# Performance work log

Measured on AMD Instinct MI355X. Metric: run time of the kernel, lower is better.

The kernel has to match this reference:

```python
import jax, jax.numpy as jnp
import numpy as np

L, D, H, DH, S, B, V = 8, 1024, 16, 64, 1024, 4, 32000
EPS = 1e-5


def layernorm(x, s, b):
    m = x.mean(-1, keepdims=True)
    v = ((x - m) ** 2).mean(-1, keepdims=True)
    return (x - m) * jax.lax.rsqrt(v + EPS) * s + b


def setup_inputs() -> dict:
    key = jax.random.key(0)
    ks = jax.random.split(key, 12)
    sd = 0.02
    inp = {
        'idx': jax.random.randint(ks[0], (B, S), 0, V),
        'tok_emb': jax.random.normal(ks[1], (V, D), jnp.float32) * sd,
        'pos_emb': jax.random.normal(ks[2], (S, D), jnp.float32) * sd,
        'ln1_s': jnp.ones((L, D), jnp.float32),
        'ln1_b': jnp.zeros((L, D), jnp.float32),
        'wq': jax.random.normal(ks[3], (L, H, D, DH), jnp.float32) * sd,
        'wk': jax.random.normal(ks[4], (L, H, D, DH), jnp.float32) * sd,
        'wv': jax.random.normal(ks[5], (L, H, D, DH), jnp.float32) * sd,
        'wproj': jax.random.normal(ks[6], (L, D, D), jnp.float32) * sd,  # stored [D_in, D_out]
        'ln2_s': jnp.ones((L, D), jnp.float32),
        'ln2_b': jnp.zeros((L, D), jnp.float32),
        'w1': jax.random.normal(ks[7], (L, D, 4 * D), jnp.float32) * sd,
        'b1': jnp.zeros((L, 4 * D), jnp.float32),
        'w2': jax.random.normal(ks[8], (L, 4 * D, D), jnp.float32) * sd,
        'b2': jnp.zeros((L, D), jnp.float32),
        'lnf_s': jnp.ones((D,), jnp.float32),
        'lnf_b': jnp.zeros((D,), jnp.float32),
        'lm_w': jax.random.normal(ks[9], (D, V), jnp.float32) * sd,  # stored [D_in, V]
        'lm_b': jnp.zeros((V,), jnp.float32),
    }
    return inp


def reference(idx, tok_emb, pos_emb, ln1_s, ln1_b, wq, wk, wv, wproj,
              ln2_s, ln2_b, w1, b1, w2, b2, lnf_s, lnf_b, lm_w, lm_b):
    T = idx.shape[1]
    x = tok_emb[idx] + pos_emb[:T]  # [B,T,D]
    mask = jnp.tril(jnp.ones((T, T), bool))
    scale = DH ** -0.5
    for l in range(L):  # fixed small layer count
        h = layernorm(x, ln1_s[l], ln1_b[l])
        q = jnp.einsum('bsd,hde->bhse', h, wq[l])
        k = jnp.einsum('bsd,hde->bhse', h, wk[l])
        v = jnp.einsum('bsd,hde->bhse', h, wv[l])
        att = jnp.einsum('bhse,bhte->bhst', q, k) * scale
        att = jnp.where(mask, att, -jnp.inf)
        att = jax.nn.softmax(att, axis=-1)  # dropout=0.0 -> identity
        o = jnp.einsum('bhst,bhte->bhse', att, v)
        o = o.transpose(0, 2, 1, 3).reshape(x.shape)  # concat heads: [B,T,H*DH]
        x = x + o @ wproj[l]
        h2 = layernorm(x, ln2_s[l], ln2_b[l])
        x = x + jax.nn.relu(h2 @ w1[l] + b1[l]) @ w2[l] + b2[l]
    x = layernorm(x, lnf_s, lnf_b)
    logits = x @ lm_w + lm_b  # [B,T,V]
    return logits
```

## Files before the change

kernel.cpp:

```cpp
#include <hip/hip_runtime.h>
#include <hip/hip_bf16.h>

#define LL 8
#define DD 1024
#define HH 16
#define DHH 64
#define SS 1024
#define BB 4
#define VV 32000
#define MM (BB * SS)

typedef unsigned short u16;
typedef __attribute__((ext_vector_type(8))) short short8v;
typedef __attribute__((ext_vector_type(4))) float f32x4;
typedef unsigned int __attribute__((address_space(1))) guint;
typedef unsigned int __attribute__((address_space(3))) luint;

__device__ __forceinline__ float bf2f_lo(unsigned u) { return __uint_as_float(u << 16); }
__device__ __forceinline__ u16 f2bf(float f) {
  unsigned x = __float_as_uint(f);
  return (u16)((x + 0x7fffu + ((x >> 16) & 1u)) >> 16);
}

__global__ __launch_bounds__(256) void embed_kernel(
    const int* __restrict__ idx, const float* __restrict__ tok,
    const float* __restrict__ pos, float* __restrict__ x) {
  int i = blockIdx.x * blockDim.x + threadIdx.x;
  int elem = i * 4;
  int row = elem / DD;
  int d = elem % DD;
  int s = row % SS;
  int t = idx[row];
  float4 tv = *(const float4*)(tok + (size_t)t * DD + d);
  float4 pv = *(const float4*)(pos + (size_t)s * DD + d);
  tv.x += pv.x; tv.y += pv.y; tv.z += pv.z; tv.w += pv.w;
  *(float4*)(x + (size_t)elem) = tv;
}

__global__ __launch_bounds__(256) void ln_bf16_kernel(
    const float* __restrict__ x, const float* __restrict__ sc,
    const float* __restrict__ bi, u16* __restrict__ out) {
  const int row = blockIdx.x;
  const int tid = threadIdx.x;
  __shared__ float red[4];
  float4 v = ((const float4*)(x + (size_t)row * DD))[tid];
  float s = v.x + v.y + v.z + v.w;
  #pragma unroll
  for (int off = 32; off; off >>= 1) s += __shfl_down(s, off);
  if ((tid & 63) == 0) red[tid >> 6] = s;
  __syncthreads();
  float mean = (red[0] + red[1] + red[2] + red[3]) * (1.f / DD);
  float dx = v.x - mean, dy = v.y - mean, dz = v.z - mean, dw = v.w - mean;
  float vs = dx * dx + dy * dy + dz * dz + dw * dw;
  __syncthreads();
  #pragma unroll
  for (int off = 32; off; off >>= 1) vs += __shfl_down(vs, off);
  if ((tid & 63) == 0) red[tid >> 6] = vs;
  __syncthreads();
  float var = (red[0] + red[1] + red[2] + red[3]) * (1.f / DD);
  float rstd = rsqrtf(var + 1e-5f);
  float4 s4 = ((const float4*)sc)[tid];
  float4 b4 = ((const float4*)bi)[tid];
  ushort4 o;
  o.x = f2bf(dx * rstd * s4.x + b4.x);
  o.y = f2bf(dy * rstd * s4.y + b4.y);
  o.z = f2bf(dz * rstd * s4.z + b4.z);
  o.w = f2bf(dw * rstd * s4.w + b4.w);
  *(ushort4*)(out + (size_t)row * DD + tid * 4) = o;
}

template <bool HEADW>
__global__ __launch_bounds__(256) void convT_kernel(
    const float* __restrict__ W, u16* __restrict__ BT, int K, int N,
    size_t lstride) {
  __shared__ float tile[32][33];
  const int n0 = blockIdx.x * 32, k0 = blockIdx.y * 32, l = blockIdx.z;
  const int tx = threadIdx.x & 31, ty = threadIdx.x >> 5;
  const float* Wl;
  int ld;
  if (HEADW) {
    const int h = n0 >> 6;
    Wl = W + ((size_t)(l * HH + h) * K) * 64 + (n0 & 63);
    ld = 64;
  } else {
    Wl = W + (size_t)l * K * N + n0;
    ld = N;
  }
  #pragma unroll
  for (int i = 0; i < 4; ++i)
    tile[ty + 8 * i][tx] = Wl[(size_t)(k0 + ty + 8 * i) * ld + tx];
  __syncthreads();
  u16* out = BT + (size_t)l * lstride;
  #pragma unroll
  for (int i = 0; i < 4; ++i)
    out[(size_t)(n0 + ty + 8 * i) * K + k0 + tx] = f2bf(tile[tx][ty + 8 * i]);
}

template <bool BIAS, bool RELU, bool RESID, bool OBF16>
__global__ __launch_bounds__(256) void gemm_mfma(
    const u16* __restrict__ A, const u16* __restrict__ BT,
    const float* __restrict__ bias, const float* __restrict__ resid,
    void* __restrict__ Cv, int M, int N, int K) {
  __shared__ u16 As[128 * 64];
  __shared__ u16 Bs[128 * 64];
  const int tid = threadIdx.x;
  const int lane = tid & 63, wave = tid >> 6;
  const int m0 = blockIdx.x * 128, n0 = blockIdx.y * 128;
  const int wr = (wave >> 1) * 64, wc = (wave & 1) * 64;
  const int srow = tid >> 3;
  const int scol = (((tid & 7) ^ (srow & 7)) * 8);
  const u16* Ag = A + (size_t)(m0 + srow) * K + scol;
  const u16* Bg = BT + (size_t)(n0 + srow) * K + scol;

  f32x4 acc[4][4] = {};
  for (int k0 = 0; k0 < K; k0 += 64) {
    #pragma unroll
    for (int c = 0; c < 4; ++c) {
      __builtin_amdgcn_global_load_lds(
          (const guint*)(Ag + k0 + (size_t)c * 32 * K),
          (luint*)(As + c * 2048 + tid * 8), 16, 0, 0);
      __builtin_amdgcn_global_load_lds(
          (const guint*)(Bg + k0 + (size_t)c * 32 * K),
          (luint*)(Bs + c * 2048 + tid * 8), 16, 0, 0);
    }
    __syncthreads();
    #pragma unroll
    for (int kk = 0; kk < 64; kk += 32) {
      const int chA = (((kk >> 3) | (lane >> 4)) ^ (lane & 7)) * 8;
      short8v av[4], bv[4];
      #pragma unroll
      for (int i = 0; i < 4; ++i)
        av[i] = *(const short8v*)(As + (wr + i * 16 + (lane & 15)) * 64 + chA);
      #pragma unroll
      for (int j = 0; j < 4; ++j)
        bv[j] = *(const short8v*)(Bs + (wc + j * 16 + (lane & 15)) * 64 + chA);
      #pragma unroll
      for (int i = 0; i < 4; ++i)
        #pragma unroll
        for (int j = 0; j < 4; ++j)
          acc[i][j] = __builtin_amdgcn_mfma_f32_16x16x32_bf16(av[i], bv[j], acc[i][j], 0, 0, 0);
    }
    __syncthreads();
  }
  #pragma unroll
  for (int i = 0; i < 4; ++i) {
    #pragma unroll
    for (int j = 0; j < 4; ++j) {
      const int col = n0 + wc + j * 16 + (lane & 15);
      #pragma unroll
      for (int r = 0; r < 4; ++r) {
        const int row = m0 + wr + i * 16 + (lane >> 4) * 4 + r;
        float v = acc[i][j][r];
        if (BIAS) v += bias[col];
        if (RELU) v = fmaxf(v, 0.f);
        if (RESID) v += resid[(size_t)row * N + col];
        if (OBF16)
          ((u16*)Cv)[(size_t)row * N + col] = f2bf(v);
        else
          ((float*)Cv)[(size_t)row * N + col] = v;
      }
    }
  }
}

#define LDA_(BUF, KH, F) \
  (*(const short8v*)&As[BUF][KH][(wm * 128 + (F) * 16 + (lane & 15)) * 32 + rg])
#define LDB_(BUF, KH, NF) \
  (*(const short8v*)&Bs[BUF][KH][(wn * 64 + (NF) * 16 + (lane & 15)) * 32 + rg])
#define LDS_A(S0,S1,S2,S3, BUF, KH, FB) { \
  S0 = LDA_(BUF, KH, (FB) + 0); S1 = LDA_(BUF, KH, (FB) + 1); \
  S2 = LDA_(BUF, KH, (FB) + 2); S3 = LDA_(BUF, KH, (FB) + 3); }
#define LDS_B(S0,S1,S2,S3, BUF, KH) { \
  S0 = LDB_(BUF, KH, 0); S1 = LDB_(BUF, KH, 1); \
  S2 = LDB_(BUF, KH, 2); S3 = LDB_(BUF, KH, 3); }
#define STAGE_A(BUF, KH, KT) do { \
  __builtin_amdgcn_global_load_lds((const guint*)(Abase + (KT) * 64 + (KH) * 32), \
      (luint*)(&As[BUF][KH][tid * 8]), 16, 0, 0); \
  __builtin_amdgcn_global_load_lds((const guint*)(Abase + (size_t)128 * K + (KT) * 64 + (KH) * 32), \
      (luint*)(&As[BUF][KH][(tid + 512) * 8]), 16, 0, 0); \
} while (0)
#define STAGE_B(BUF, KH, KT) do { \
  __builtin_amdgcn_global_load_lds((const guint*)(Bbase + (KT) * 64 + (KH) * 32), \
      (luint*)(&Bs[BUF][KH][tid * 8]), 16, 0, 0); \
  __builtin_amdgcn_global_load_lds((const guint*)(Bbase + (size_t)128 * K + (KT) * 64 + (KH) * 32), \
      (luint*)(&Bs[BUF][KH][(tid + 512) * 8]), 16, 0, 0); \
} while (0)
#define MROW(F, AQ, B0,B1,B2,B3) \
  acc[F][0] = __builtin_amdgcn_mfma_f32_16x16x32_bf16(AQ, B0, acc[F][0], 0, 0, 0); \
  acc[F][1] = __builtin_amdgcn_mfma_f32_16x16x32_bf16(AQ, B1, acc[F][1], 0, 0, 0); \
  acc[F][2] = __builtin_amdgcn_mfma_f32_16x16x32_bf16(AQ, B2, acc[F][2], 0, 0, 0); \
  acc[F][3] = __builtin_amdgcn_mfma_f32_16x16x32_bf16(AQ, B3, acc[F][3], 0, 0, 0);
#define MFMA16S(FB, A0,A1,A2,A3, B0,B1,B2,B3) \
  MROW((FB) + 0, A0, B0,B1,B2,B3) MROW((FB) + 1, A1, B0,B1,B2,B3) \
  MROW((FB) + 2, A2, B0,B1,B2,B3) MROW((FB) + 3, A3, B0,B1,B2,B3)
#define BARRIER __builtin_amdgcn_s_barrier()
#define MEMFENCE asm volatile("" ::: "memory")

#define TILE4(CUR, KT, ST1, ST2, V1STR, V3STR, LD4, LGK4STR) { \
  const int cur_ = (CUR); \
   \
  MEMFENCE; \
  LDS_A(aN0,aN1,aN2,aN3, cur_, 0, 4); \
  if (ST1) { STAGE_A(cur_ ^ 1, 1, (KT) + 1); } \
  asm volatile("s_waitcnt " V1STR ::: "memory"); \
  asm volatile("s_waitcnt lgkmcnt(4)" ::: "memory"); \
  BARRIER; \
  __builtin_amdgcn_s_setprio(1); \
  MFMA16S(0, aP0,aP1,aP2,aP3, bP0,bP1,bP2,bP3); \
  __builtin_amdgcn_s_setprio(0); \
   \
  MEMFENCE; \
  LDS_A(aP0,aP1,aP2,aP3, cur_, 1, 0); \
  LDS_B(bN0,bN1,bN2,bN3, cur_, 1); \
  if (ST1) { STAGE_B(cur_ ^ 1, 1, (KT) + 1); } \
  asm volatile("s_waitcnt lgkmcnt(8)" ::: "memory"); \
  BARRIER; \
  __builtin_amdgcn_s_setprio(1); \
  MFMA16S(4, aN0,aN1,aN2,aN3, bP0,bP1,bP2,bP3); \
  __builtin_amdgcn_s_setprio(0); \
   \
  MEMFENCE; \
  LDS_A(aN0,aN1,aN2,aN3, cur_, 1, 4); \
  if (ST2) { STAGE_A(cur_, 0, (KT) + 2); } \
  asm volatile("s_waitcnt " V3STR ::: "memory"); \
  asm volatile("s_waitcnt lgkmcnt(4)" ::: "memory"); \
  BARRIER; \
  __builtin_amdgcn_s_setprio(1); \
  MFMA16S(0, aP0,aP1,aP2,aP3, bN0,bN1,bN2,bN3); \
  __builtin_amdgcn_s_setprio(0); \
   \
  MEMFENCE; \
  if (LD4) { LDS_A(aP0,aP1,aP2,aP3, cur_ ^ 1, 0, 0); \
             LDS_B(bP0,bP1,bP2,bP3, cur_ ^ 1, 0); } \
  if (ST2) { STAGE_B(cur_, 0, (KT) + 2); } \
  asm volatile("s_waitcnt " LGK4STR ::: "memory"); \
  BARRIER; \
  __builtin_amdgcn_s_setprio(1); \
  MFMA16S(4, aN0,aN1,aN2,aN3, bN0,bN1,bN2,bN3); \
  __builtin_amdgcn_s_setprio(0); \
}

template <bool BIAS, bool RELU, bool RESID, bool OBF16>
__global__ __launch_bounds__(512, 2) void gemm8(
    const u16* __restrict__ A, const u16* __restrict__ BT,
    const float* __restrict__ bias, const float* __restrict__ resid,
    void* __restrict__ Cv, int M, int N, int K) {
  __shared__ u16 As[2][2][8192];
  __shared__ u16 Bs[2][2][8192];
  const int tid = threadIdx.x;
  const int lane = tid & 63, wave = tid >> 6;
  const int wm = wave >> 2, wn = wave & 3;
  const int nwg = gridDim.x;
  const int bid = blockIdx.x;
  const int wg = ((nwg & 7) == 0) ? ((bid & 7) * (nwg >> 3) + (bid >> 3)) : bid;
  const int nmt = M >> 8;
  const int m0 = (wg % nmt) * 256;
  const int n0 = (wg / nmt) * 256;
  const int NT = K >> 6;
  const int sr = tid >> 2;
  const int ssc = (((tid & 3) ^ ((tid >> 3) & 3)) * 8);
  const u16* Abase = A + (size_t)(m0 + sr) * K + ssc;
  const u16* Bbase = BT + (size_t)(n0 + sr) * K + ssc;
  const int rg = (((lane >> 4) ^ ((lane >> 1) & 3)) * 8);

  f32x4 acc[8][4] = {};
  short8v aP0, aP1, aP2, aP3, aN0, aN1, aN2, aN3;
  short8v bP0, bP1, bP2, bP3, bN0, bN1, bN2, bN3;

  STAGE_A(0, 0, 0); STAGE_B(0, 0, 0);
  STAGE_A(0, 1, 0); STAGE_B(0, 1, 0);
  STAGE_A(1, 0, 1); STAGE_B(1, 0, 1);
  asm volatile("s_waitcnt vmcnt(8)" ::: "memory");
  BARRIER;
  MEMFENCE;
  LDS_A(aP0,aP1,aP2,aP3, 0, 0, 0);
  LDS_B(bP0,bP1,bP2,bP3, 0, 0);

  int kt = 0;
  for (; kt < NT - 2; ++kt) {
    TILE4(kt & 1, kt, true, true, "vmcnt(6)", "vmcnt(6)", true, "lgkmcnt(8)");
  }
  TILE4(kt & 1, kt, true, false, "vmcnt(6)", "vmcnt(4)", true, "lgkmcnt(8)");
  ++kt;
  TILE4(kt & 1, kt, false, false, "vmcnt(0)", "vmcnt(0)", false, "lgkmcnt(0)");

  #pragma unroll
  for (int f = 0; f < 8; ++f) {
    #pragma unroll
    for (int n = 0; n < 4; ++n) {
      const int col = n0 + wn * 64 + n * 16 + (lane & 15);
      #pragma unroll
      for (int r = 0; r < 4; ++r) {
        const int row = m0 + wm * 128 + f * 16 + (lane >> 4) * 4 + r;
        float v = acc[f][n][r];
        if (BIAS) v += bias[col];
        if (RELU) v = fmaxf(v, 0.f);
        if (RESID) v += resid[(size_t)row * N + col];
        if (OBF16)
          ((u16*)Cv)[(size_t)row * N + col] = f2bf(v);
        else
          ((float*)Cv)[(size_t)row * N + col] = v;
      }
    }
  }
}

__global__ __launch_bounds__(256) void gemm_fb(
    const u16* __restrict__ A, const float* __restrict__ B,
    const float* __restrict__ bias, float* __restrict__ C, int M, int N, int K) {
  __shared__ alignas(16) float Asm[16][68];
  __shared__ alignas(16) float Bsm[16][68];
  const int tid = threadIdx.x;
  const int tx = tid & 15, ty = tid >> 4;
  const int m0 = blockIdx.y * 64, n0 = blockIdx.x * 64;
  const int ar = tid >> 2, ac = (tid & 3) * 4;
  const int br = tid >> 4, bc = (tid & 15) * 4;
  float acc[4][4] = {};
  for (int k0 = 0; k0 < K; k0 += 16) {
    ushort4 au = *(const ushort4*)(A + (size_t)(m0 + ar) * K + k0 + ac);
    float4 bv = *(const float4*)(B + (size_t)(k0 + br) * N + n0 + bc);
    Asm[ac + 0][ar] = bf2f_lo(au.x);
    Asm[ac + 1][ar] = bf2f_lo(au.y);
    Asm[ac + 2][ar] = bf2f_lo(au.z);
    Asm[ac + 3][ar] = bf2f_lo(au.w);
    *(float4*)&Bsm[br][bc] = bv;
    __syncthreads();
    #pragma unroll
    for (int kk = 0; kk < 16; ++kk) {
      float4 a = *(const float4*)&Asm[kk][ty * 4];
      float4 b = *(const float4*)&Bsm[kk][tx * 4];
      acc[0][0] += a.x * b.x; acc[0][1] += a.x * b.y; acc[0][2] += a.x * b.z; acc[0][3] += a.x * b.w;
      acc[1][0] += a.y * b.x; acc[1][1] += a.y * b.y; acc[1][2] += a.y * b.z; acc[1][3] += a.y * b.w;
      acc[2][0] += a.z * b.x; acc[2][1] += a.z * b.y; acc[2][2] += a.z * b.z; acc[2][3] += a.z * b.w;
      acc[3][0] += a.w * b.x; acc[3][1] += a.w * b.y; acc[3][2] += a.w * b.z; acc[3][3] += a.w * b.w;
    }
    __syncthreads();
  }
  #pragma unroll
  for (int i = 0; i < 4; ++i) {
    const int m = m0 + ty * 4 + i;
    #pragma unroll
    for (int j = 0; j < 4; ++j) {
      const int n = n0 + tx * 4 + j;
      C[(size_t)m * N + n] = acc[i][j] + bias[n];
    }
  }
}

__global__ __launch_bounds__(256) void attn_mfma(
    const u16* __restrict__ qk, const u16* __restrict__ vt,
    u16* __restrict__ o) {
  __shared__ alignas(16) u16 Ksh[64 * 64];
  __shared__ alignas(16) u16 Vsh[64 * 64];
  __shared__ unsigned Plds[4][16 * 41];
  __shared__ float bcast[4][16];
  const int tid = threadIdx.x;
  const int lane = tid & 63, wave = tid >> 6;
  const int g = lane >> 4, qi = lane & 15;
  const int qt = blockIdx.x, h = blockIdx.y, b = blockIdx.z;
  const int q0w = qt * 64 + wave * 16;
  const int qloc = wave * 16 + qi;

  short8v qf0, qf1;
  {
    const u16* qp = qk + ((size_t)b * SS + q0w + qi) * 2048 + h * DHH + g * 8;
    qf0 = *(const short8v*)qp;
    qf1 = *(const short8v*)(qp + 32);
  }

  f32x4 oacc[4] = {};
  float mrow = -1e30f, lrow = 0.f;

  for (int kt = 0; kt <= qt; ++kt) {
    __syncthreads();
    #pragma unroll
    for (int u = 0; u < 2; ++u) {
      const int unit = tid + 256 * u;
      const int row = unit >> 3, ch = unit & 7;
      const int sch = ch ^ (row & 7);
      __builtin_amdgcn_global_load_lds(
          (const guint*)(qk + ((size_t)b * SS + kt * 64 + row) * 2048 + 1024 + h * DHH + sch * 8),
          (luint*)(Ksh + unit * 8), 16, 0, 0);
      __builtin_amdgcn_global_load_lds(
          (const guint*)(vt + ((size_t)(h * DHH + row)) * MM + b * SS + kt * 64 + sch * 8),
          (luint*)(Vsh + unit * 8), 16, 0, 0);
    }
    __syncthreads();

    f32x4 st[4] = {};
    #pragma unroll
    for (int t = 0; t < 4; ++t) {
      const int row = t * 16 + qi;
      const int swz = (row & 7) << 4;
      short8v kf0 = *(const short8v*)(Ksh + row * 64 + (((g * 16) ^ swz) >> 1));
      short8v kf1 = *(const short8v*)(Ksh + row * 64 + (((64 + g * 16) ^ swz) >> 1));
      st[t] = __builtin_amdgcn_mfma_f32_16x16x32_bf16(kf0, qf0, st[t], 0, 0, 0);
      st[t] = __builtin_amdgcn_mfma_f32_16x16x32_bf16(kf1, qf1, st[t], 0, 0, 0);
    }

    if (kt == qt) {
      #pragma unroll
      for (int t = 0; t < 4; ++t)
        #pragma unroll
        for (int r = 0; r < 4; ++r)
          if (t * 16 + 4 * g + r > qloc) st[t][r] = -1e30f;
    }

    float mt = st[0][0];
    #pragma unroll
    for (int t = 0; t < 4; ++t)
      #pragma unroll
      for (int r = 0; r < 4; ++r) mt = fmaxf(mt, st[t][r]);
    mt = fmaxf(mt, __shfl_xor(mt, 16));
    mt = fmaxf(mt, __shfl_xor(mt, 32));
    const float mnew = fmaxf(mrow, mt * 0.125f);
    const float corr = __expf(mrow - mnew);
    float pl = 0.f;
    #pragma unroll
    for (int t = 0; t < 4; ++t) {
      #pragma unroll
      for (int r2 = 0; r2 < 2; ++r2) {
        float plo = __expf(fmaf(st[t][2 * r2], 0.125f, -mnew));
        float phi = __expf(fmaf(st[t][2 * r2 + 1], 0.125f, -mnew));
        pl += plo + phi;
        Plds[wave][qi * 41 + 8 * t + 2 * g + r2] =
            (unsigned)f2bf(plo) | ((unsigned)f2bf(phi) << 16);
      }
    }
    pl += __shfl_xor(pl, 16);
    pl += __shfl_xor(pl, 32);
    lrow = lrow * corr + pl;
    mrow = mnew;

    if (g == 0) bcast[wave][qi] = corr;
    float c0 = bcast[wave][g * 4 + 0];
    float c1 = bcast[wave][g * 4 + 1];
    float c2 = bcast[wave][g * 4 + 2];
    float c3 = bcast[wave][g * 4 + 3];
    #pragma unroll
    for (int dvt = 0; dvt < 4; ++dvt) {
      oacc[dvt][0] *= c0; oacc[dvt][1] *= c1;
      oacc[dvt][2] *= c2; oacc[dvt][3] *= c3;
    }

    union U8 { unsigned u[4]; short8v s8; };
    U8 pa0, pa1;
    #pragma unroll
    for (int c = 0; c < 4; ++c) {
      pa0.u[c] = Plds[wave][qi * 41 + g * 4 + c];
      pa1.u[c] = Plds[wave][qi * 41 + 16 + g * 4 + c];
    }
    #pragma unroll
    for (int dvt = 0; dvt < 4; ++dvt) {
      const int row = dvt * 16 + qi;
      const int swz = (row & 7) << 4;
      short8v v0 = *(const short8v*)(Vsh + row * 64 + (((g * 16) ^ swz) >> 1));
      short8v v1 = *(const short8v*)(Vsh + row * 64 + (((64 + g * 16) ^ swz) >> 1));
      oacc[dvt] = __builtin_amdgcn_mfma_f32_16x16x32_bf16(pa0.s8, v0, oacc[dvt], 0, 0, 0);
      oacc[dvt] = __builtin_amdgcn_mfma_f32_16x16x32_bf16(pa1.s8, v1, oacc[dvt], 0, 0, 0);
    }
  }

  if (g == 0) bcast[wave][qi] = 1.f / lrow;
  float i0 = bcast[wave][g * 4 + 0];
  float i1 = bcast[wave][g * 4 + 1];
  float i2 = bcast[wave][g * 4 + 2];
  float i3 = bcast[wave][g * 4 + 3];
  #pragma unroll
  for (int dvt = 0; dvt < 4; ++dvt) {
    const int col = h * DHH + dvt * 16 + qi;
    o[((size_t)b * SS + q0w + g * 4 + 0) * DD + col] = f2bf(oacc[dvt][0] * i0);
    o[((size_t)b * SS + q0w + g * 4 + 1) * DD + col] = f2bf(oacc[dvt][1] * i1);
    o[((size_t)b * SS + q0w + g * 4 + 2) * DD + col] = f2bf(oacc[dvt][2] * i2);
    o[((size_t)b * SS + q0w + g * 4 + 3) * DD + col] = f2bf(oacc[dvt][3] * i3);
  }
}

extern "C" void kernel_launch(void* const* d_in, const int* in_sizes, int n_in,
                              void* d_out, int out_size, void* d_ws, size_t ws_size,
                              hipStream_t stream) {
  const int* idx = (const int*)d_in[0];
  const float* tok_emb = (const float*)d_in[1];
  const float* pos_emb = (const float*)d_in[2];
  const float* ln1_s = (const float*)d_in[3];
  const float* ln1_b = (const float*)d_in[4];
  const float* wq = (const float*)d_in[5];
  const float* wk = (const float*)d_in[6];
  const float* wv = (const float*)d_in[7];
  const float* wproj = (const float*)d_in[8];
  const float* ln2_s = (const float*)d_in[9];
  const float* ln2_b = (const float*)d_in[10];
  const float* w1 = (const float*)d_in[11];
  const float* b1 = (const float*)d_in[12];
  const float* w2 = (const float*)d_in[13];
  const float* b2 = (const float*)d_in[14];
  const float* lnf_s = (const float*)d_in[15];
  const float* lnf_b = (const float*)d_in[16];
  const float* lm_w = (const float*)d_in[17];
  const float* lm_b = (const float*)d_in[18];

  const size_t MD = (size_t)MM * DD;

  u16* sc0 = (u16*)d_out;
  u16* BTqk = sc0;
  u16* BTv = BTqk + (size_t)LL * 2048 * DD;
  u16* BTp = BTv + (size_t)LL * DD * DD;
  u16* BTw1 = BTp + (size_t)LL * DD * DD;
  u16* BTw2 = BTw1 + (size_t)LL * DD * 4 * DD;
  u16* qkb = BTw2 + (size_t)LL * DD * 4 * DD;
  u16* vtb = qkb + (size_t)MM * 2048;
  u16* ob = vtb + MD;
  u16* tmp = ob + MD;

  float* x = (float*)d_ws;
  u16* h = (u16*)((char*)d_ws + MD * 4);
  u16* BTlm = (u16*)((char*)d_ws + MD * 4 + MD * 2);
  const bool big_ws = ws_size >= (MD * 4 + MD * 2 + (size_t)VV * DD * 2);

  const dim3 blk(256);

  convT_kernel<true><<<dim3(DD / 32, DD / 32, LL), blk, 0, stream>>>(
      wq, BTqk, DD, DD, (size_t)2048 * DD);
  convT_kernel<true><<<dim3(DD / 32, DD / 32, LL), blk, 0, stream>>>(
      wk, BTqk + (size_t)DD * DD, DD, DD, (size_t)2048 * DD);
  convT_kernel<true><<<dim3(DD / 32, DD / 32, LL), blk, 0, stream>>>(
      wv, BTv, DD, DD, (size_t)DD * DD);
  convT_kernel<false><<<dim3(DD / 32, DD / 32, LL), blk, 0, stream>>>(
      wproj, BTp, DD, DD, (size_t)DD * DD);
  convT_kernel<false><<<dim3(4 * DD / 32, DD / 32, LL), blk, 0, stream>>>(
      w1, BTw1, DD, 4 * DD, (size_t)DD * 4 * DD);
  convT_kernel<false><<<dim3(DD / 32, 4 * DD / 32, LL), blk, 0, stream>>>(
      w2, BTw2, 4 * DD, DD, (size_t)4 * DD * DD);
  if (big_ws)
    convT_kernel<false><<<dim3(VV / 32, DD / 32, 1), blk, 0, stream>>>(
        lm_w, BTlm, DD, VV, (size_t)VV * DD);

  embed_kernel<<<(MM * DD / 4 + 255) / 256, blk, 0, stream>>>(idx, tok_emb, pos_emb, x);

  for (int l = 0; l < LL; ++l) {
    ln_bf16_kernel<<<MM, blk, 0, stream>>>(x, ln1_s + l * DD, ln1_b + l * DD, h);
    gemm8<false, false, false, true><<<dim3((MM / 256) * (2048 / 256)), dim3(512), 0, stream>>>(
        h, BTqk + (size_t)l * 2048 * DD, nullptr, nullptr, qkb, MM, 2048, DD);
    gemm_mfma<false, false, false, true><<<dim3(DD / 128, MM / 128), blk, 0, stream>>>(
        BTv + (size_t)l * DD * DD, h, nullptr, nullptr, vtb, DD, MM, DD);
    attn_mfma<<<dim3(SS / 64, HH, BB), blk, 0, stream>>>(qkb, vtb, ob);
    gemm_mfma<false, false, true, false><<<dim3(MM / 128, DD / 128), blk, 0, stream>>>(
        ob, BTp + (size_t)l * DD * DD, nullptr, x, x, MM, DD, DD);
    ln_bf16_kernel<<<MM, blk, 0, stream>>>(x, ln2_s + l * DD, ln2_b + l * DD, h);
    gemm8<true, true, false, true><<<dim3((MM / 256) * (4 * DD / 256)), dim3(512), 0, stream>>>(
        h, BTw1 + (size_t)l * DD * 4 * DD, b1 + (size_t)l * 4 * DD, nullptr, tmp,
        MM, 4 * DD, DD);
    gemm_mfma<true, false, true, false><<<dim3(MM / 128, DD / 128), blk, 0, stream>>>(
        tmp, BTw2 + (size_t)l * 4 * DD * DD, b2 + (size_t)l * DD, x, x, MM, DD, 4 * DD);
  }

  ln_bf16_kernel<<<MM, blk, 0, stream>>>(x, lnf_s, lnf_b, h);
  if (big_ws) {
    gemm8<true, false, false, false><<<dim3((MM / 256) * (VV / 256)), dim3(512), 0, stream>>>(
        h, BTlm, lm_b, nullptr, (float*)d_out, MM, VV, DD);
  } else {
    gemm_fb<<<dim3(VV / 64, MM / 64), blk, 0, stream>>>(
        h, lm_w, lm_b, (float*)d_out, MM, VV, DD);
  }
}
```

Measured before the change: 2.714 ms.

## Fuse QKV projection into one GEMM, transpose V separately, add nontemporal stores

Concatenates the Q, K and V weight transposes into a single 3072-wide B matrix. The projection now runs as one gemm8 launch instead of a gemm8 plus a separate gemm_mfma for V. A new transpose_v kernel builds the V^T layout that attention expects, and the attention kernel now reads Q and K with a 3072 stride. Separately, nontemporal stores are added for the FFN1 output, the LM-head logits and the fallback GEMM output, to reduce cache pollution; the extra transpose pass costs additional memory traffic.

After: 2.621 ms. 3.4% less time.

```diff
diff --git a/kernel.cpp b/kernel.cpp
--- a/kernel.cpp
+++ b/kernel.cpp
@@ -94,6 +94,20 @@
   #pragma unroll
   for (int i = 0; i < 4; ++i)
     out[(size_t)(n0 + ty + 8 * i) * K + k0 + tx] = f2bf(tile[tx][ty + 8 * i]);
+}
+
+__global__ __launch_bounds__(256) void transpose_v(
+    const u16* __restrict__ qkv, u16* __restrict__ vt) {
+  __shared__ u16 t[32][33];
+  const int s0 = blockIdx.x * 32, d0 = blockIdx.y * 32;
+  const int tx = threadIdx.x & 31, ty = threadIdx.x >> 5;
+  #pragma unroll
+  for (int i = 0; i < 4; ++i)
+    t[ty + 8 * i][tx] = qkv[(size_t)(s0 + ty + 8 * i) * 3072 + 2048 + d0 + tx];
+  __syncthreads();
+  #pragma unroll
+  for (int i = 0; i < 4; ++i)
+    vt[(size_t)(d0 + ty + 8 * i) * MM + s0 + tx] = t[tx][ty + 8 * i];
 }
 
 template <bool BIAS, bool RELU, bool RESID, bool OBF16>
@@ -198,7 +212,6 @@
 
 #define TILE4(CUR, KT, ST1, ST2, V1STR, V3STR, LD4, LGK4STR) { \
   const int cur_ = (CUR); \
-   \
   MEMFENCE; \
   LDS_A(aN0,aN1,aN2,aN3, cur_, 0, 4); \
   if (ST1) { STAGE_A(cur_ ^ 1, 1, (KT) + 1); } \
@@ -208,7 +221,6 @@
   __builtin_amdgcn_s_setprio(1); \
   MFMA16S(0, aP0,aP1,aP2,aP3, bP0,bP1,bP2,bP3); \
   __builtin_amdgcn_s_setprio(0); \
-   \
   MEMFENCE; \
   LDS_A(aP0,aP1,aP2,aP3, cur_, 1, 0); \
   LDS_B(bN0,bN1,bN2,bN3, cur_, 1); \
@@ -218,7 +230,6 @@
   __builtin_amdgcn_s_setprio(1); \
   MFMA16S(4, aN0,aN1,aN2,aN3, bP0,bP1,bP2,bP3); \
   __builtin_amdgcn_s_setprio(0); \
-   \
   MEMFENCE; \
   LDS_A(aN0,aN1,aN2,aN3, cur_, 1, 4); \
   if (ST2) { STAGE_A(cur_, 0, (KT) + 2); } \
@@ -228,7 +239,6 @@
   __builtin_amdgcn_s_setprio(1); \
   MFMA16S(0, aP0,aP1,aP2,aP3, bN0,bN1,bN2,bN3); \
   __builtin_amdgcn_s_setprio(0); \
-   \
   MEMFENCE; \
   if (LD4) { LDS_A(aP0,aP1,aP2,aP3, cur_ ^ 1, 0, 0); \
              LDS_B(bP0,bP1,bP2,bP3, cur_ ^ 1, 0); } \
@@ -240,7 +250,7 @@
   __builtin_amdgcn_s_setprio(0); \
 }
 
-template <bool BIAS, bool RELU, bool RESID, bool OBF16>
+template <bool BIAS, bool RELU, bool RESID, bool OBF16, bool NTC>
 __global__ __launch_bounds__(512, 2) void gemm8(
     const u16* __restrict__ A, const u16* __restrict__ BT,
     const float* __restrict__ bias, const float* __restrict__ resid,
@@ -296,10 +306,14 @@
         if (BIAS) v += bias[col];
         if (RELU) v = fmaxf(v, 0.f);
         if (RESID) v += resid[(size_t)row * N + col];
-        if (OBF16)
-          ((u16*)Cv)[(size_t)row * N + col] = f2bf(v);
-        else
-          ((float*)Cv)[(size_t)row * N + col] = v;
+        if (OBF16) {
+          u16 val = f2bf(v);
+          if (NTC) __builtin_nontemporal_store(val, &((u16*)Cv)[(size_t)row * N + col]);
+          else ((u16*)Cv)[(size_t)row * N + col] = val;
+        } else {
+          if (NTC) __builtin_nontemporal_store(v, &((float*)Cv)[(size_t)row * N + col]);
+          else ((float*)Cv)[(size_t)row * N + col] = v;
+        }
       }
     }
   }
@@ -342,13 +356,13 @@
     #pragma unroll
     for (int j = 0; j < 4; ++j) {
       const int n = n0 + tx * 4 + j;
-      C[(size_t)m * N + n] = acc[i][j] + bias[n];
+      __builtin_nontemporal_store(acc[i][j] + bias[n], &C[(size_t)m * N + n]);
     }
   }
 }
 
 __global__ __launch_bounds__(256) void attn_mfma(
-    const u16* __restrict__ qk, const u16* __restrict__ vt,
+    const u16* __restrict__ qkv, const u16* __restrict__ vt,
     u16* __restrict__ o) {
   __shared__ alignas(16) u16 Ksh[64 * 64];
   __shared__ alignas(16) u16 Vsh[64 * 64];
@@ -363,7 +377,7 @@
 
   short8v qf0, qf1;
   {
-    const u16* qp = qk + ((size_t)b * SS + q0w + qi) * 2048 + h * DHH + g * 8;
+    const u16* qp = qkv + ((size_t)b * SS + q0w + qi) * 3072 + h * DHH + g * 8;
     qf0 = *(const short8v*)qp;
     qf1 = *(const short8v*)(qp + 32);
   }
@@ -379,7 +393,7 @@
       const int row = unit >> 3, ch = unit & 7;
       const int sch = ch ^ (row & 7);
       __builtin_amdgcn_global_load_lds(
-          (const guint*)(qk + ((size_t)b * SS + kt * 64 + row) * 2048 + 1024 + h * DHH + sch * 8),
+          (const guint*)(qkv + ((size_t)b * SS + kt * 64 + row) * 3072 + 1024 + h * DHH + sch * 8),
           (luint*)(Ksh + unit * 8), 16, 0, 0);
       __builtin_amdgcn_global_load_lds(
           (const guint*)(vt + ((size_t)(h * DHH + row)) * MM + b * SS + kt * 64 + sch * 8),
@@ -502,13 +516,12 @@
   const size_t MD = (size_t)MM * DD;
 
   u16* sc0 = (u16*)d_out;
-  u16* BTqk = sc0;
-  u16* BTv = BTqk + (size_t)LL * 2048 * DD;
-  u16* BTp = BTv + (size_t)LL * DD * DD;
+  u16* BTqkv = sc0;
+  u16* BTp = BTqkv + (size_t)LL * 3072 * DD;
   u16* BTw1 = BTp + (size_t)LL * DD * DD;
   u16* BTw2 = BTw1 + (size_t)LL * DD * 4 * DD;
-  u16* qkb = BTw2 + (size_t)LL * DD * 4 * DD;
-  u16* vtb = qkb + (size_t)MM * 2048;
+  u16* qkvb = BTw2 + (size_t)LL * DD * 4 * DD;
+  u16* vtb = qkvb + (size_t)MM * 3072;
   u16* ob = vtb + MD;
   u16* tmp = ob + MD;
 
@@ -520,11 +533,11 @@
   const dim3 blk(256);
 
   convT_kernel<true><<<dim3(DD / 32, DD / 32, LL), blk, 0, stream>>>(
-      wq, BTqk, DD, DD, (size_t)2048 * DD);
+      wq, BTqkv, DD, DD, (size_t)3072 * DD);
   convT_kernel<true><<<dim3(DD / 32, DD / 32, LL), blk, 0, stream>>>(
-      wk, BTqk + (size_t)DD * DD, DD, DD, (size_t)2048 * DD);
+      wk, BTqkv + (size_t)DD * DD, DD, DD, (size_t)3072 * DD);
   convT_kernel<true><<<dim3(DD / 32, DD / 32, LL), blk, 0, stream>>>(
-      wv, BTv, DD, DD, (size_t)DD * DD);
+      wv, BTqkv + (size_t)2 * DD * DD, DD, DD, (size_t)3072 * DD);
   convT_kernel<false><<<dim3(DD / 32, DD / 32, LL), blk, 0, stream>>>(
       wproj, BTp, DD, DD, (size_t)DD * DD);
   convT_kernel<false><<<dim3(4 * DD / 32, DD / 32, LL), blk, 0, stream>>>(
@@ -539,15 +552,14 @@
 
   for (int l = 0; l < LL; ++l) {
     ln_bf16_kernel<<<MM, blk, 0, stream>>>(x, ln1_s + l * DD, ln1_b + l * DD, h);
-    gemm8<false, false, false, true><<<dim3((MM / 256) * (2048 / 256)), dim3(512), 0, stream>>>(
-        h, BTqk + (size_t)l * 2048 * DD, nullptr, nullptr, qkb, MM, 2048, DD);
-    gemm_mfma<false, false, false, true><<<dim3(DD / 128, MM / 128), blk, 0, stream>>>(
-        BTv + (size_t)l * DD * DD, h, nullptr, nullptr, vtb, DD, MM, DD);
-    attn_mfma<<<dim3(SS / 64, HH, BB), blk, 0, stream>>>(qkb, vtb, ob);
+    gemm8<false, false, false, true, false><<<dim3((MM / 256) * (3072 / 256)), dim3(512), 0, stream>>>(
+        h, BTqkv + (size_t)l * 3072 * DD, nullptr, nullptr, qkvb, MM, 3072, DD);
+    transpose_v<<<dim3(MM / 32, DD / 32), blk, 0, stream>>>(qkvb, vtb);
+    attn_mfma<<<dim3(SS / 64, HH, BB), blk, 0, stream>>>(qkvb, vtb, ob);
     gemm_mfma<false, false, true, false><<<dim3(MM / 128, DD / 128), blk, 0, stream>>>(
         ob, BTp + (size_t)l * DD * DD, nullptr, x, x, MM, DD, DD);
     ln_bf16_kernel<<<MM, blk, 0, stream>>>(x, ln2_s + l * DD, ln2_b + l * DD, h);
-    gemm8<true, true, false, true><<<dim3((MM / 256) * (4 * DD / 256)), dim3(512), 0, stream>>>(
+    gemm8<true, true, false, true, true><<<dim3((MM / 256) * (4 * DD / 256)), dim3(512), 0, stream>>>(
         h, BTw1 + (size_t)l * DD * 4 * DD, b1 + (size_t)l * 4 * DD, nullptr, tmp,
         MM, 4 * DD, DD);
     gemm_mfma<true, false, true, false><<<dim3(MM / 128, DD / 128), blk, 0, stream>>>(
@@ -556,7 +568,7 @@
 
   ln_bf16_kernel<<<MM, blk, 0, stream>>>(x, lnf_s, lnf_b, h);
   if (big_ws) {
-    gemm8<true, false, false, false><<<dim3((MM / 256) * (VV / 256)), dim3(512), 0, stream>>>(
+    gemm8<true, false, false, false, true><<<dim3((MM / 256) * (VV / 256)), dim3(512), 0, stream>>>(
         h, BTlm, lm_b, nullptr, (float*)d_out, MM, VV, DD);
   } else {
     gemm_fb<<<dim3(VV / 64, MM / 64), blk, 0, stream>>>(
```
